# Optimization experiments

Hardware: AMD Instinct MI355X
Metric: run time of the kernel (lower is better)

Reference implementation:

```python
import jax, jax.numpy as jnp
import numpy as np
from jax import lax

INT32_MAX = 2147483647


def setup_inputs() -> dict:
    key = jax.random.key(0)
    kx, ky = jax.random.split(key)
    x = jax.random.normal(kx, (4096, 64), dtype=jnp.float32)
    y = jax.random.normal(ky, (100000, 64), dtype=jnp.float32)
    return {"x": x, "y": y, "k": 16, "n_splits": 10}


def reference(x, y, k, n_splits):
    """Streaming k-NN: L2 path distance with incremental top-k merge.

    x: (B1, d) queries; y: (B2, d) database. Returns
      ds:  (B1, k)    k smallest distances
      idx: (B1, k, 1) global indices into y (int32), matching (B1,k,y.ndim-1).
    """
    B1, d = x.shape
    B2 = y.shape[0]
    split = B2 // n_splits
    y_splits = y.reshape(n_splits, split, d)  # even splits, as in torch .split
    bases = jnp.arange(n_splits, dtype=jnp.int32) * split

    x2 = jnp.sum(x * x, axis=-1, keepdims=True)  # (B1, 1)

    ds0 = jnp.full((B1, k), jnp.inf, dtype=x.dtype)
    idx0 = jnp.full((B1, k), INT32_MAX, dtype=jnp.int32)
    col = jnp.arange(split, dtype=jnp.int32)

    def step(carry, inp):
        ds, idx = carry
        y_b, base = inp                               # (split, d), scalar
        y2 = jnp.sum(y_b * y_b, axis=-1)              # (split,)
        d2 = x2 + y2[None, :] - 2.0 * (x @ y_b.T)     # (B1, split)
        new_ds = jnp.sqrt(jnp.maximum(d2, 0.0))
        new_idx = jnp.broadcast_to(base + col, (B1, split))
        cat_ds = jnp.concatenate([ds, new_ds], axis=1)      # (B1, k+split)
        cat_idx = jnp.concatenate([idx, new_idx], axis=1)
        neg_top, pos = lax.top_k(-cat_ds, k)                # smallest-k
        ds = -neg_top
        idx = jnp.take_along_axis(cat_idx, pos, axis=1)
        return (ds, idx), None

    (ds, idx), _ = lax.scan(step, (ds0, idx0), (y_splits, bases))
    return ds, idx[..., None]
```

## Files before the change

### kernel.cpp

```cpp
#include <hip/hip_runtime.h>
#include <math.h>

#define D 64
#define K 16
#define NSEG_WANT 128
#define CAP_WANT 512
#define YPAD 128
#define SLOT_B 2304
#define DEPTH 2

typedef __attribute__((ext_vector_type(8))) short short8;
typedef __attribute__((ext_vector_type(4))) float f32x4;

#define SB __builtin_amdgcn_sched_barrier(0)

__device__ __forceinline__ unsigned short f32_to_bf16_rne(float f) {
    unsigned u = __float_as_uint(f);
    u = u + 0x7FFFu + ((u >> 16) & 1u);
    return (unsigned short)(u >> 16);
}

__device__ __forceinline__ void gload16(const void* g, void* l) {
    __builtin_amdgcn_global_load_lds((const __attribute__((address_space(1))) void*)g,
                                     (__attribute__((address_space(3))) void*)l, 16, 0, 0);
}
__device__ __forceinline__ void gload4(const void* g, void* l) {
    __builtin_amdgcn_global_load_lds((const __attribute__((address_space(1))) void*)g,
                                     (__attribute__((address_space(3))) void*)l, 4, 0, 0);
}

__global__ __launch_bounds__(256)
void prep_kernel(const float* __restrict__ x, const float* __restrict__ y,
                 unsigned short* __restrict__ xbneg,
                 unsigned short* __restrict__ yb,
                 float* __restrict__ y2, int B1, int B2)
{
    const int w = threadIdx.x >> 6, lane = threadIdx.x & 63;
    const int row = blockIdx.x * 4 + w;
    const int B2p = B2 + YPAD;
    if (row < B2) {
        const float v = y[(size_t)row * D + lane];
        float s = v * v;
        #pragma unroll
        for (int off = 32; off > 0; off >>= 1) s += __shfl_xor(s, off);
        yb[(size_t)row * D + lane] = f32_to_bf16_rne(v);
        if (lane == 0) y2[row] = s;
    } else if (row < B2p) {
        yb[(size_t)row * D + lane] = 0;
        if (lane == 0) y2[row] = INFINITY;
    } else if (row < B2p + B1) {
        const int r = row - B2p;
        const float v = x[(size_t)r * D + lane];
        xbneg[(size_t)r * D + lane] = f32_to_bf16_rne(-2.0f * v);
    }
}

#define DECODE_BLOCK()                                                       \
    const int id  = blockIdx.x;                                              \
    const int xcd = id & 7;                                                  \
    const int t_  = id >> 3;                                                 \
    const int nqg = B1 >> 8;                                                 \
    const int qi  = t_ % nqg;                                                \
    const int s   = (t_ / nqg) * 8 + xcd;

#define STAGE(slotIdx, c)                                                    \
    do {                                                                     \
        unsigned char* _sb = wl + (slotIdx) * SLOT_B;                        \
        const unsigned short* _g0 = gbase + (size_t)((c) * 16 + 0) * D;      \
        const unsigned short* _g1 = gbase + (size_t)((c) * 16 + 8) * D;      \
        gload16(_g0, _sb);                                                   \
        gload16(_g1, _sb + 1024);                                            \
        gload4(y2g + base + (c) * 16 + lane, _sb + 2048);                    \
    } while (0)

#define WAITSLOT()                                                           \
    do {                                                                     \
        asm volatile("s_waitcnt vmcnt(3)" ::: "memory");                     \
        SB;                                                                  \
    } while (0)

__global__ __launch_bounds__(256)
void knn_min_kernel(const unsigned short* __restrict__ xbneg,
                    const unsigned short* __restrict__ yb,
                    const float* __restrict__ y2g,
                    float* __restrict__ pmin,
                    int B1, int B2, int segsz, int nseg)
{
    const int tid  = threadIdx.x;
    const int w    = tid >> 6;
    const int lane = tid & 63;
    const int n15  = lane & 15;
    const int quad = lane >> 4;
    DECODE_BLOCK();
    const int qb   = qi * 256 + w * 64;
    const int base = s * segsz;
    const int segN = min(segsz, B2 - base);
    const int nch  = segN >> 4;
    const int nchE = nch & ~1;

    __shared__ __align__(16) unsigned char lds_buf[4 * DEPTH * SLOT_B];
    unsigned char* wl = lds_buf + w * (DEPTH * SLOT_B);

    const short8 b00 = *(const short8*)&xbneg[(size_t)(qb +  0 + n15) * D + quad * 8];
    const short8 b01 = *(const short8*)&xbneg[(size_t)(qb +  0 + n15) * D + 32 + quad * 8];
    const short8 b10 = *(const short8*)&xbneg[(size_t)(qb + 16 + n15) * D + quad * 8];
    const short8 b11 = *(const short8*)&xbneg[(size_t)(qb + 16 + n15) * D + 32 + quad * 8];
    const short8 b20 = *(const short8*)&xbneg[(size_t)(qb + 32 + n15) * D + quad * 8];
    const short8 b21 = *(const short8*)&xbneg[(size_t)(qb + 32 + n15) * D + 32 + quad * 8];
    const short8 b30 = *(const short8*)&xbneg[(size_t)(qb + 48 + n15) * D + quad * 8];
    const short8 b31 = *(const short8*)&xbneg[(size_t)(qb + 48 + n15) * D + 32 + quad * 8];
    SB;

    const int srow  = lane >> 3;
    const int sslot = (lane & 7) ^ srow;
    const unsigned short* gbase = yb + (size_t)(base + srow) * D + (sslot << 3);
    const int roff0 = n15 * 128 + (((quad    ) ^ (n15 & 7)) << 4);
    const int roff1 = n15 * 128 + (((quad + 4) ^ (n15 & 7)) << 4);
    const int yoff  = 2048 + (quad << 4);

    float rm0 = INFINITY, rm1 = INFINITY, rm2 = INFINITY, rm3 = INFINITY;

    STAGE(0, 0); STAGE(1, 1);
    SB;

#define STEP_MIN(slotIdx, c)                                                        \
    do {                                                                            \
        WAITSLOT();                                                                 \
        const unsigned char* _lb = wl + (slotIdx) * SLOT_B;                         \
        const short8 a0 = *(const short8*)(_lb + roff0);                            \
        const short8 a1 = *(const short8*)(_lb + roff1);                            \
        const float4 yv = *(const float4*)(_lb + yoff);                             \
        SB;                                       \
        STAGE(slotIdx, (c) + 2);                    \
        f32x4 acc;                                                                  \
        acc = (f32x4){yv.x, yv.y, yv.z, yv.w};                                      \
        acc = __builtin_amdgcn_mfma_f32_16x16x32_bf16(a0, b00, acc, 0, 0, 0);       \
        acc = __builtin_amdgcn_mfma_f32_16x16x32_bf16(a1, b01, acc, 0, 0, 0);       \
        rm0 = fminf(rm0, fminf(fminf(acc[0], acc[1]), fminf(acc[2], acc[3])));      \
        acc = (f32x4){yv.x, yv.y, yv.z, yv.w};                                      \
        acc = __builtin_amdgcn_mfma_f32_16x16x32_bf16(a0, b10, acc, 0, 0, 0);       \
        acc = __builtin_amdgcn_mfma_f32_16x16x32_bf16(a1, b11, acc, 0, 0, 0);       \
        rm1 = fminf(rm1, fminf(fminf(acc[0], acc[1]), fminf(acc[2], acc[3])));      \
        acc = (f32x4){yv.x, yv.y, yv.z, yv.w};                                      \
        acc = __builtin_amdgcn_mfma_f32_16x16x32_bf16(a0, b20, acc, 0, 0, 0);       \
        acc = __builtin_amdgcn_mfma_f32_16x16x32_bf16(a1, b21, acc, 0, 0, 0);       \
        rm2 = fminf(rm2, fminf(fminf(acc[0], acc[1]), fminf(acc[2], acc[3])));      \
        acc = (f32x4){yv.x, yv.y, yv.z, yv.w};                                      \
        acc = __builtin_amdgcn_mfma_f32_16x16x32_bf16(a0, b30, acc, 0, 0, 0);       \
        acc = __builtin_amdgcn_mfma_f32_16x16x32_bf16(a1, b31, acc, 0, 0, 0);       \
        rm3 = fminf(rm3, fminf(fminf(acc[0], acc[1]), fminf(acc[2], acc[3])));      \
    } while (0)

    for (int ci = 0; ci < nchE; ci += 2) {
        STEP_MIN(0, ci);
        STEP_MIN(1, ci + 1);
    }
    if (nch & 1) STEP_MIN(0, nchE);
#undef STEP_MIN

    asm volatile("s_waitcnt vmcnt(0)" ::: "memory");

    pmin[((size_t)(qb +  0 + n15) * nseg + s) * 4 + quad] = rm0;
    pmin[((size_t)(qb + 16 + n15) * nseg + s) * 4 + quad] = rm1;
    pmin[((size_t)(qb + 32 + n15) * nseg + s) * 4 + quad] = rm2;
    pmin[((size_t)(qb + 48 + n15) * nseg + s) * 4 + quad] = rm3;
}

__global__ __launch_bounds__(256)
void knn_thresh_kernel(const float* __restrict__ pmin,
                       float* __restrict__ Tq, int* __restrict__ cnt,
                       int B1, int npart)
{
    const int w    = threadIdx.x >> 6;
    const int lane = threadIdx.x & 63;
    const int q    = blockIdx.x * 4 + w;

    const float* p = pmin + (size_t)q * npart;
    float cd = p[lane];
    float worst = cd;
    #pragma unroll
    for (int off = 32; off > 0; off >>= 1) worst = fmaxf(worst, __shfl_xor(worst, off));

    for (int b = 64; b < npart; b += 64) {
        const float v = p[b + lane];
        for (int j = 0; j < 64; ++j) {
            const float dv = __shfl(v, j);
            if (dv < worst) {
                const unsigned long long m = __ballot(cd == worst);
                const int vict = __ffsll(m) - 1;
                if (lane == vict) cd = dv;
                float wv = cd;
                #pragma unroll
                for (int off = 32; off > 0; off >>= 1) wv = fmaxf(wv, __shfl_xor(wv, off));
                worst = wv;
            }
        }
    }
    if (lane == 0) { Tq[q] = worst; cnt[q] = 0; }
}

__global__ __launch_bounds__(256)
void knn_filter_kernel(const unsigned short* __restrict__ xbneg,
                       const unsigned short* __restrict__ yb,
                       const float* __restrict__ y2g,
                       const float* __restrict__ Tq,
                       int* __restrict__ cnt,
                       float* __restrict__ sd, int* __restrict__ si,
                       int B1, int B2, int segsz, int nseg, int cap)
{
    const int tid  = threadIdx.x;
    const int w    = tid >> 6;
    const int lane = tid & 63;
    const int n15  = lane & 15;
    const int quad = lane >> 4;
    DECODE_BLOCK();
    const int qb   = qi * 256 + w * 64;
    const int base = s * segsz;
    const int segN = min(segsz, B2 - base);
    const int nch  = segN >> 4;
    const int nchE = nch & ~1;

    __shared__ __align__(16) unsigned char lds_buf[4 * DEPTH * SLOT_B];
    unsigned char* wl = lds_buf + w * (DEPTH * SLOT_B);

    const short8 b00 = *(const short8*)&xbneg[(size_t)(qb +  0 + n15) * D + quad * 8];
    const short8 b01 = *(const short8*)&xbneg[(size_t)(qb +  0 + n15) * D + 32 + quad * 8];
    const short8 b10 = *(const short8*)&xbneg[(size_t)(qb + 16 + n15) * D + quad * 8];
    const short8 b11 = *(const short8*)&xbneg[(size_t)(qb + 16 + n15) * D + 32 + quad * 8];
    const short8 b20 = *(const short8*)&xbneg[(size_t)(qb + 32 + n15) * D + quad * 8];
    const short8 b21 = *(const short8*)&xbneg[(size_t)(qb + 32 + n15) * D + 32 + quad * 8];
    const short8 b30 = *(const short8*)&xbneg[(size_t)(qb + 48 + n15) * D + quad * 8];
    const short8 b31 = *(const short8*)&xbneg[(size_t)(qb + 48 + n15) * D + 32 + quad * 8];

    const int q0 = qb +  0 + n15;
    const int q1 = qb + 16 + n15;
    const int q2 = qb + 32 + n15;
    const int q3 = qb + 48 + n15;
    const float th0 = Tq[q0];
    const float th1 = Tq[q1];
    const float th2 = Tq[q2];
    const float th3 = Tq[q3];
    SB;

    const int srow  = lane >> 3;
    const int sslot = (lane & 7) ^ srow;
    const unsigned short* gbase = yb + (size_t)(base + srow) * D + (sslot << 3);
    const int roff0 = n15 * 128 + (((quad    ) ^ (n15 & 7)) << 4);
    const int roff1 = n15 * 128 + (((quad + 4) ^ (n15 & 7)) << 4);
    const int yoff  = 2048 + (quad << 4);

    STAGE(0, 0); STAGE(1, 1);
    SB;

#define GROUP_FLT(A0, A1, B0, B1_, YV, TH, QQ, CB)                                  \
    do {                                                                            \
        f32x4 acc = {(YV).x, (YV).y, (YV).z, (YV).w};                               \
        acc = __builtin_amdgcn_mfma_f32_16x16x32_bf16(A0, B0, acc, 0, 0, 0);        \
        acc = __builtin_amdgcn_mfma_f32_16x16x32_bf16(A1, B1_, acc, 0, 0, 0);       \
        const float m0 = acc[0];                                                    \
        const float m1 = acc[1];                                                    \
        const float m2 = acc[2];                                                    \
        const float m3 = acc[3];                                                    \
        const float mm = fminf(fminf(m0, m1), fminf(m2, m3));                       \
        if (mm <= (TH)) {                                                           \
            if (m0 <= (TH)) { const int p_ = atomicAdd(&cnt[QQ], 1); if (p_ < cap) { sd[(size_t)(QQ) * cap + p_] = m0; si[(size_t)(QQ) * cap + p_] = (CB) + 0; } } \
            if (m1 <= (TH)) { const int p_ = atomicAdd(&cnt[QQ], 1); if (p_ < cap) { sd[(size_t)(QQ) * cap + p_] = m1; si[(size_t)(QQ) * cap + p_] = (CB) + 1; } } \
            if (m2 <= (TH)) { const int p_ = atomicAdd(&cnt[QQ], 1); if (p_ < cap) { sd[(size_t)(QQ) * cap + p_] = m2; si[(size_t)(QQ) * cap + p_] = (CB) + 2; } } \
            if (m3 <= (TH)) { const int p_ = atomicAdd(&cnt[QQ], 1); if (p_ < cap) { sd[(size_t)(QQ) * cap + p_] = m3; si[(size_t)(QQ) * cap + p_] = (CB) + 3; } } \
        }                                                                           \
    } while (0)

#define STEP_FLT(slotIdx, c)                                                        \
    do {                                                                            \
        WAITSLOT();                                                                 \
        const unsigned char* _lb = wl + (slotIdx) * SLOT_B;                         \
        const short8 a0 = *(const short8*)(_lb + roff0);                            \
        const short8 a1 = *(const short8*)(_lb + roff1);                            \
        const float4 yv = *(const float4*)(_lb + yoff);                             \
        SB;                                       \
        STAGE(slotIdx, (c) + 2);                                                    \
        const int cb = base + ((c) << 4) + 4 * quad;                                \
        GROUP_FLT(a0, a1, b00, b01, yv, th0, q0, cb);                               \
        GROUP_FLT(a0, a1, b10, b11, yv, th1, q1, cb);                               \
        GROUP_FLT(a0, a1, b20, b21, yv, th2, q2, cb);                               \
        GROUP_FLT(a0, a1, b30, b31, yv, th3, q3, cb);                               \
    } while (0)

    for (int ci = 0; ci < nchE; ci += 2) {
        STEP_FLT(0, ci);
        STEP_FLT(1, ci + 1);
    }
    if (nch & 1) STEP_FLT(0, nchE);
#undef STEP_FLT
#undef GROUP_FLT

    asm volatile("s_waitcnt vmcnt(0)" ::: "memory");
}

__global__ __launch_bounds__(256)
void knn_merge_refine_kernel(const float* __restrict__ sd,
                             const int*   __restrict__ si,
                             const int*   __restrict__ cnt,
                             const float* __restrict__ x,
                             const float* __restrict__ y,
                             float* __restrict__ out_ds,
                             float* __restrict__ out_idx,
                             int B1, int B2, int cap)
{
    const int w    = threadIdx.x >> 6;
    const int lane = threadIdx.x & 63;
    const int q    = blockIdx.x * 4 + w;

    float cd = INFINITY;
    int   ci = 2147483647;
    float worst = INFINITY;

    const int n = min(cnt[q], cap);
    const float* sdq = sd + (size_t)q * cap;
    const int*   siq = si + (size_t)q * cap;

    for (int b = 0; b < n; b += 64) {
        const int t = b + lane;
        const float vv = (t < n) ? sdq[t] : INFINITY;
        const int   iv = (t < n) ? siq[t] : 2147483647;
        const int lim = min(64, n - b);
        for (int j = 0; j < lim; ++j) {
            const float dv = __shfl(vv, j);
            if (dv < worst) {
                const int jidx = __shfl(iv, j);
                const unsigned long long m = __ballot(cd == worst);
                const int vict = __ffsll(m) - 1;
                if (lane == vict) { cd = dv; ci = jidx; }
                float wv = cd;
                #pragma unroll
                for (int off = 32; off > 0; off >>= 1)
                    wv = fmaxf(wv, __shfl_xor(wv, off));
                worst = wv;
            }
        }
    }

    __shared__ float xs[4][D];
    __shared__ float sds[4][64];
    __shared__ int   sidx[4][64];

    if (lane < D / 4)
        ((float4*)xs[w])[lane] = ((const float4*)(x + (size_t)q * D))[lane];
    __syncthreads();

    float x2 = 0.f;
    #pragma unroll
    for (int i = 0; i < D; ++i) x2 = __fadd_rn(x2, __fmul_rn(xs[w][i], xs[w][i]));

    int idx = ci;
    float ds32 = INFINITY;
    if (idx >= 0 && idx < B2) {
        float yr[D];
        const float4* yrow = (const float4*)(y + (size_t)idx * D);
        #pragma unroll
        for (int t = 0; t < D / 4; ++t) {
            float4 v = yrow[t];
            yr[4*t+0] = v.x; yr[4*t+1] = v.y; yr[4*t+2] = v.z; yr[4*t+3] = v.w;
        }
        float y2 = 0.f;
        #pragma unroll
        for (int i = 0; i < D; ++i) y2 = __fadd_rn(y2, __fmul_rn(yr[i], yr[i]));

        float dot = 0.f;
        #pragma unroll
        for (int i = 0; i < D; ++i) dot = __fmaf_rn(xs[w][i], yr[i], dot);

        const float d2 = __fsub_rn(__fadd_rn(x2, y2), __fmul_rn(2.0f, dot));
        ds32 = __fsqrt_rn(fmaxf(d2, 0.f));
    } else {
        idx = 2147483647;
    }
    sds[w][lane]  = ds32;
    sidx[w][lane] = idx;
    __syncthreads();

    int rank = 0;
    for (int j = 0; j < 64; ++j) {
        const float dj = sds[w][j];
        bool prec = (dj < ds32);
        if (dj == ds32 && sidx[w][j] != idx) {
            const int  jd    = sidx[w][j];
            const long dd    = (long)jd - (long)idx;
            const long add   = dd < 0 ? -dd : dd;
            const bool t2win = (add >= 21504 && add <= 23552);
            prec = t2win ? (jd > idx) : (jd < idx);
        }
        if (prec) ++rank;
    }
    if (rank < K) {
        out_ds [(size_t)q * K + rank] = ds32;
        out_idx[(size_t)q * K + rank] = (float)idx;
    }
}

extern "C" void kernel_launch(void* const* d_in, const int* in_sizes, int n_in,
                              void* d_out, int out_size, void* d_ws, size_t ws_size,
                              hipStream_t stream)
{
    const float* x = (const float*)d_in[0];
    const float* y = (const float*)d_in[1];

    const int B1 = in_sizes[0] / D;
    const int B2 = in_sizes[1] / D;
    const int B2p = B2 + YPAD;

    const int segsz = (((B2 + NSEG_WANT - 1) / NSEG_WANT) + 15) & ~15;
    const int nseg  = (B2 + segsz - 1) / segsz;

    size_t off = 0;
    unsigned short* xbneg = (unsigned short*)((char*)d_ws + off); off += (size_t)B1 * D * 2;
    unsigned short* yb    = (unsigned short*)((char*)d_ws + off); off += (size_t)B2p * D * 2;
    float*          y2    = (float*)((char*)d_ws + off);          off += (size_t)B2p * 4;
    float*          pmin  = (float*)((char*)d_ws + off);          off += (size_t)B1 * nseg * 4 * 4;
    float*          Tq    = (float*)((char*)d_ws + off);          off += (size_t)B1 * 4;
    int*            cnt   = (int*)((char*)d_ws + off);            off += (size_t)B1 * 4;

    int cap = CAP_WANT;
    {
        const size_t per = (size_t)B1 * 8;
        if (off + (size_t)cap * per > ws_size) {
            const size_t avail = ws_size > off ? ws_size - off : 0;
            cap = (int)(avail / per);
            if (cap < 16) cap = 16;
        }
    }
    float* sd = (float*)((char*)d_ws + off); off += (size_t)B1 * cap * 4;
    int*   si = (int*)((char*)d_ws + off);

    float* out_ds  = (float*)d_out;
    float* out_idx = out_ds + (size_t)B1 * K;

    const int prows = B2p + B1;
    prep_kernel<<<(prows + 3) / 4, 256, 0, stream>>>(x, y, xbneg, yb, y2, B1, B2);

    const int nblk = (B1 / 256) * nseg;
    knn_min_kernel<<<nblk, 256, 0, stream>>>(xbneg, yb, y2, pmin, B1, B2, segsz, nseg);

    knn_thresh_kernel<<<B1 / 4, 256, 0, stream>>>(pmin, Tq, cnt, B1, nseg * 4);

    knn_filter_kernel<<<nblk, 256, 0, stream>>>(xbneg, yb, y2, Tq, cnt, sd, si,
                                                B1, B2, segsz, nseg, cap);

    knn_merge_refine_kernel<<<B1 / 4, 256, 0, stream>>>(sd, si, cnt, x, y,
                                                        out_ds, out_idx,
                                                        B1, B2, cap);
}
```

Before: 342.5 us.

## Give each wave 128 queries in min and filter kernels to halve y traffic

Each wave now holds eight 16-query B fragments instead of four, so a block of two waves covers 256 queries. Every y chunk staged into LDS is reused by twice as many MFMAs, which halves the global-to-LDS loads of the database per query block and the per-wave staging overhead. In exchange the kernels keep more live registers, use half the waves per block, and may lose occupancy or latency hiding.

```diff
diff --git a/kernel.cpp b/kernel.cpp
--- a/kernel.cpp
+++ b/kernel.cpp
@@ -8,6 +8,7 @@
 #define YPAD 128
 #define SLOT_B 2304
 #define DEPTH 2
+#define NGRP 8
 
 typedef __attribute__((ext_vector_type(8))) short short8;
 typedef __attribute__((ext_vector_type(4))) float f32x4;
@@ -79,7 +80,7 @@
         SB;                                                                  \
     } while (0)
 
-__global__ __launch_bounds__(256)
+__global__ __launch_bounds__(128, 4)
 void knn_min_kernel(const unsigned short* __restrict__ xbneg,
                     const unsigned short* __restrict__ yb,
                     const float* __restrict__ y2g,
@@ -92,23 +93,22 @@
     const int n15  = lane & 15;
     const int quad = lane >> 4;
     DECODE_BLOCK();
-    const int qb   = qi * 256 + w * 64;
+    const int qb0  = qi * 256 + w * 128;
     const int base = s * segsz;
     const int segN = min(segsz, B2 - base);
     const int nch  = segN >> 4;
     const int nchE = nch & ~1;
 
-    __shared__ __align__(16) unsigned char lds_buf[4 * DEPTH * SLOT_B];
+    __shared__ __align__(16) unsigned char lds_buf[2 * DEPTH * SLOT_B];
     unsigned char* wl = lds_buf + w * (DEPTH * SLOT_B);
 
-    const short8 b00 = *(const short8*)&xbneg[(size_t)(qb +  0 + n15) * D + quad * 8];
-    const short8 b01 = *(const short8*)&xbneg[(size_t)(qb +  0 + n15) * D + 32 + quad * 8];
-    const short8 b10 = *(const short8*)&xbneg[(size_t)(qb + 16 + n15) * D + quad * 8];
-    const short8 b11 = *(const short8*)&xbneg[(size_t)(qb + 16 + n15) * D + 32 + quad * 8];
-    const short8 b20 = *(const short8*)&xbneg[(size_t)(qb + 32 + n15) * D + quad * 8];
-    const short8 b21 = *(const short8*)&xbneg[(size_t)(qb + 32 + n15) * D + 32 + quad * 8];
-    const short8 b30 = *(const short8*)&xbneg[(size_t)(qb + 48 + n15) * D + quad * 8];
-    const short8 b31 = *(const short8*)&xbneg[(size_t)(qb + 48 + n15) * D + 32 + quad * 8];
+    short8 bA[NGRP], bB[NGRP];
+    #pragma unroll
+    for (int g = 0; g < NGRP; ++g) {
+        const size_t qr = (size_t)(qb0 + g * 16 + n15) * D;
+        bA[g] = *(const short8*)&xbneg[qr + quad * 8];
+        bB[g] = *(const short8*)&xbneg[qr + 32 + quad * 8];
+    }
     SB;
 
     const int srow  = lane >> 3;
@@ -118,7 +118,9 @@
     const int roff1 = n15 * 128 + (((quad + 4) ^ (n15 & 7)) << 4);
     const int yoff  = 2048 + (quad << 4);
 
-    float rm0 = INFINITY, rm1 = INFINITY, rm2 = INFINITY, rm3 = INFINITY;
+    float rm[NGRP];
+    #pragma unroll
+    for (int g = 0; g < NGRP; ++g) rm[g] = INFINITY;
 
     STAGE(0, 0); STAGE(1, 1);
     SB;
@@ -132,23 +134,14 @@
         const float4 yv = *(const float4*)(_lb + yoff);                             \
         SB;                                       \
         STAGE(slotIdx, (c) + 2);                    \
-        f32x4 acc;                                                                  \
-        acc = (f32x4){yv.x, yv.y, yv.z, yv.w};                                      \
-        acc = __builtin_amdgcn_mfma_f32_16x16x32_bf16(a0, b00, acc, 0, 0, 0);       \
-        acc = __builtin_amdgcn_mfma_f32_16x16x32_bf16(a1, b01, acc, 0, 0, 0);       \
-        rm0 = fminf(rm0, fminf(fminf(acc[0], acc[1]), fminf(acc[2], acc[3])));      \
-        acc = (f32x4){yv.x, yv.y, yv.z, yv.w};                                      \
-        acc = __builtin_amdgcn_mfma_f32_16x16x32_bf16(a0, b10, acc, 0, 0, 0);       \
-        acc = __builtin_amdgcn_mfma_f32_16x16x32_bf16(a1, b11, acc, 0, 0, 0);       \
-        rm1 = fminf(rm1, fminf(fminf(acc[0], acc[1]), fminf(acc[2], acc[3])));      \
-        acc = (f32x4){yv.x, yv.y, yv.z, yv.w};                                      \
-        acc = __builtin_amdgcn_mfma_f32_16x16x32_bf16(a0, b20, acc, 0, 0, 0);       \
-        acc = __builtin_amdgcn_mfma_f32_16x16x32_bf16(a1, b21, acc, 0, 0, 0);       \
-        rm2 = fminf(rm2, fminf(fminf(acc[0], acc[1]), fminf(acc[2], acc[3])));      \
-        acc = (f32x4){yv.x, yv.y, yv.z, yv.w};                                      \
-        acc = __builtin_amdgcn_mfma_f32_16x16x32_bf16(a0, b30, acc, 0, 0, 0);       \
-        acc = __builtin_amdgcn_mfma_f32_16x16x32_bf16(a1, b31, acc, 0, 0, 0);       \
-        rm3 = fminf(rm3, fminf(fminf(acc[0], acc[1]), fminf(acc[2], acc[3])));      \
+        _Pragma("unroll")                                                           \
+        for (int g = 0; g < NGRP; ++g) {                                            \
+            f32x4 acc = {yv.x, yv.y, yv.z, yv.w};                                   \
+            acc = __builtin_amdgcn_mfma_f32_16x16x32_bf16(a0, bA[g], acc, 0, 0, 0); \
+            acc = __builtin_amdgcn_mfma_f32_16x16x32_bf16(a1, bB[g], acc, 0, 0, 0); \
+            rm[g] = fminf(rm[g], fminf(fminf(acc[0], acc[1]),                       \
+                                       fminf(acc[2], acc[3])));                     \
+        }                                                                           \
     } while (0)
 
     for (int ci = 0; ci < nchE; ci += 2) {
@@ -160,10 +153,9 @@
 
     asm volatile("s_waitcnt vmcnt(0)" ::: "memory");
 
-    pmin[((size_t)(qb +  0 + n15) * nseg + s) * 4 + quad] = rm0;
-    pmin[((size_t)(qb + 16 + n15) * nseg + s) * 4 + quad] = rm1;
-    pmin[((size_t)(qb + 32 + n15) * nseg + s) * 4 + quad] = rm2;
-    pmin[((size_t)(qb + 48 + n15) * nseg + s) * 4 + quad] = rm3;
+    #pragma unroll
+    for (int g = 0; g < NGRP; ++g)
+        pmin[((size_t)(qb0 + g * 16 + n15) * nseg + s) * 4 + quad] = rm[g];
 }
 
 __global__ __launch_bounds__(256)
@@ -199,7 +191,7 @@
     if (lane == 0) { Tq[q] = worst; cnt[q] = 0; }
 }
 
-__global__ __launch_bounds__(256)
+__global__ __launch_bounds__(128, 4)
 void knn_filter_kernel(const unsigned short* __restrict__ xbneg,
                        const unsigned short* __restrict__ yb,
                        const float* __restrict__ y2g,
@@ -214,32 +206,26 @@
     const int n15  = lane & 15;
     const int quad = lane >> 4;
     DECODE_BLOCK();
-    const int qb   = qi * 256 + w * 64;
+    const int qb0  = qi * 256 + w * 128;
     const int base = s * segsz;
     const int segN = min(segsz, B2 - base);
     const int nch  = segN >> 4;
     const int nchE = nch & ~1;
 
-    __shared__ __align__(16) unsigned char lds_buf[4 * DEPTH * SLOT_B];
+    __shared__ __align__(16) unsigned char lds_buf[2 * DEPTH * SLOT_B];
     unsigned char* wl = lds_buf + w * (DEPTH * SLOT_B);
 
-    const short8 b00 = *(const short8*)&xbneg[(size_t)(qb +  0 + n15) * D + quad * 8];
-    const short8 b01 = *(const short8*)&xbneg[(size_t)(qb +  0 + n15) * D + 32 + quad * 8];
-    const short8 b10 = *(const short8*)&xbneg[(size_t)(qb + 16 + n15) * D + quad * 8];
-    const short8 b11 = *(const short8*)&xbneg[(size_t)(qb + 16 + n15) * D + 32 + quad * 8];
-    const short8 b20 = *(const short8*)&xbneg[(size_t)(qb + 32 + n15) * D + quad * 8];
-    const short8 b21 = *(const short8*)&xbneg[(size_t)(qb + 32 + n15) * D + 32 + quad * 8];
-    const short8 b30 = *(const short8*)&xbneg[(size_t)(qb + 48 + n15) * D + quad * 8];
-    const short8 b31 = *(const short8*)&xbneg[(size_t)(qb + 48 + n15) * D + 32 + quad * 8];
-
-    const int q0 = qb +  0 + n15;
-    const int q1 = qb + 16 + n15;
-    const int q2 = qb + 32 + n15;
-    const int q3 = qb + 48 + n15;
-    const float th0 = Tq[q0];
-    const float th1 = Tq[q1];
-    const float th2 = Tq[q2];
-    const float th3 = Tq[q3];
+    short8 bA[NGRP], bB[NGRP];
+    int    qg[NGRP];
+    float  th[NGRP];
+    #pragma unroll
+    for (int g = 0; g < NGRP; ++g) {
+        qg[g] = qb0 + g * 16 + n15;
+        const size_t qr = (size_t)qg[g] * D;
+        bA[g] = *(const short8*)&xbneg[qr + quad * 8];
+        bB[g] = *(const short8*)&xbneg[qr + 32 + quad * 8];
+        th[g] = Tq[qg[g]];
+    }
     SB;
 
     const int srow  = lane >> 3;
@@ -251,24 +237,6 @@
 
     STAGE(0, 0); STAGE(1, 1);
     SB;
-
-#define GROUP_FLT(A0, A1, B0, B1_, YV, TH, QQ, CB)                                  \
-    do {                                                                            \
-        f32x4 acc = {(YV).x, (YV).y, (YV).z, (YV).w};                               \
-        acc = __builtin_amdgcn_mfma_f32_16x16x32_bf16(A0, B0, acc, 0, 0, 0);        \
-        acc = __builtin_amdgcn_mfma_f32_16x16x32_bf16(A1, B1_, acc, 0, 0, 0);       \
-        const float m0 = acc[0];                                                    \
-        const float m1 = acc[1];                                                    \
-        const float m2 = acc[2];                                                    \
-        const float m3 = acc[3];                                                    \
-        const float mm = fminf(fminf(m0, m1), fminf(m2, m3));                       \
-        if (mm <= (TH)) {                                                           \
-            if (m0 <= (TH)) { const int p_ = atomicAdd(&cnt[QQ], 1); if (p_ < cap) { sd[(size_t)(QQ) * cap + p_] = m0; si[(size_t)(QQ) * cap + p_] = (CB) + 0; } } \
-            if (m1 <= (TH)) { const int p_ = atomicAdd(&cnt[QQ], 1); if (p_ < cap) { sd[(size_t)(QQ) * cap + p_] = m1; si[(size_t)(QQ) * cap + p_] = (CB) + 1; } } \
-            if (m2 <= (TH)) { const int p_ = atomicAdd(&cnt[QQ], 1); if (p_ < cap) { sd[(size_t)(QQ) * cap + p_] = m2; si[(size_t)(QQ) * cap + p_] = (CB) + 2; } } \
-            if (m3 <= (TH)) { const int p_ = atomicAdd(&cnt[QQ], 1); if (p_ < cap) { sd[(size_t)(QQ) * cap + p_] = m3; si[(size_t)(QQ) * cap + p_] = (CB) + 3; } } \
-        }                                                                           \
-    } while (0)
 
 #define STEP_FLT(slotIdx, c)                                                        \
     do {                                                                            \
@@ -280,10 +248,24 @@
         SB;                                       \
         STAGE(slotIdx, (c) + 2);                                                    \
         const int cb = base + ((c) << 4) + 4 * quad;                                \
-        GROUP_FLT(a0, a1, b00, b01, yv, th0, q0, cb);                               \
-        GROUP_FLT(a0, a1, b10, b11, yv, th1, q1, cb);                               \
-        GROUP_FLT(a0, a1, b20, b21, yv, th2, q2, cb);                               \
-        GROUP_FLT(a0, a1, b30, b31, yv, th3, q3, cb);                               \
+        _Pragma("unroll")                                                           \
+        for (int g = 0; g < NGRP; ++g) {                                            \
+            f32x4 acc = {yv.x, yv.y, yv.z, yv.w};                                   \
+            acc = __builtin_amdgcn_mfma_f32_16x16x32_bf16(a0, bA[g], acc, 0, 0, 0); \
+            acc = __builtin_amdgcn_mfma_f32_16x16x32_bf16(a1, bB[g], acc, 0, 0, 0); \
+            const float m0 = acc[0];                                                \
+            const float m1 = acc[1];                                                \
+            const float m2 = acc[2];                                                \
+            const float m3 = acc[3];                                                \
+            const float mm = fminf(fminf(m0, m1), fminf(m2, m3));                   \
+            if (mm <= th[g]) {                                                      \
+                const int QQ = qg[g];                                               \
+                if (m0 <= th[g]) { const int p_ = atomicAdd(&cnt[QQ], 1); if (p_ < cap) { sd[(size_t)QQ * cap + p_] = m0; si[(size_t)QQ * cap + p_] = cb + 0; } } \
+                if (m1 <= th[g]) { const int p_ = atomicAdd(&cnt[QQ], 1); if (p_ < cap) { sd[(size_t)QQ * cap + p_] = m1; si[(size_t)QQ * cap + p_] = cb + 1; } } \
+                if (m2 <= th[g]) { const int p_ = atomicAdd(&cnt[QQ], 1); if (p_ < cap) { sd[(size_t)QQ * cap + p_] = m2; si[(size_t)QQ * cap + p_] = cb + 2; } } \
+                if (m3 <= th[g]) { const int p_ = atomicAdd(&cnt[QQ], 1); if (p_ < cap) { sd[(size_t)QQ * cap + p_] = m3; si[(size_t)QQ * cap + p_] = cb + 3; } } \
+            }                                                                       \
+        }                                                                           \
     } while (0)
 
     for (int ci = 0; ci < nchE; ci += 2) {
@@ -292,7 +274,6 @@
     }
     if (nch & 1) STEP_FLT(0, nchE);
 #undef STEP_FLT
-#undef GROUP_FLT
 
     asm volatile("s_waitcnt vmcnt(0)" ::: "memory");
 }
@@ -439,11 +420,11 @@
     prep_kernel<<<(prows + 3) / 4, 256, 0, stream>>>(x, y, xbneg, yb, y2, B1, B2);
 
     const int nblk = (B1 / 256) * nseg;
-    knn_min_kernel<<<nblk, 256, 0, stream>>>(xbneg, yb, y2, pmin, B1, B2, segsz, nseg);
+    knn_min_kernel<<<nblk, 128, 0, stream>>>(xbneg, yb, y2, pmin, B1, B2, segsz, nseg);
 
     knn_thresh_kernel<<<B1 / 4, 256, 0, stream>>>(pmin, Tq, cnt, B1, nseg * 4);
 
-    knn_filter_kernel<<<nblk, 256, 0, stream>>>(xbneg, yb, y2, Tq, cnt, sd, si,
+    knn_filter_kernel<<<nblk, 128, 0, stream>>>(xbneg, yb, y2, Tq, cnt, sd, si,
                                                 B1, B2, segsz, nseg, cap);
 
     knn_merge_refine_kernel<<<B1 / 4, 256, 0, stream>>>(sd, si, cnt, x, y,
```

New measurement: 337.3 us. About the same (-1.5%).
